# Kernel optimization log

Hardware: AMD Instinct MI355X
Metric: run time of the kernel (lower is better)

## Reference

```python
import jax, jax.numpy as jnp
import numpy as np


def setup_inputs() -> dict:
    key = jax.random.key(0)
    k0, k1, k2, k3 = jax.random.split(key, 4)
    B, T, C, H = 4, 4096, 1024, 64
    input_val = jax.random.normal(k0, (B, T, C), dtype=jnp.float32)
    scale = 0.02
    Wq = jax.random.normal(k1, (H, C), dtype=jnp.float32) * scale
    Wk = jax.random.normal(k2, (H, C), dtype=jnp.float32) * scale
    Wv = jax.random.normal(k3, (H, C), dtype=jnp.float32) * scale
    k_mask = jnp.ones((B, T), dtype=jnp.int32)
    return {"input_val": input_val, "Wq": Wq, "Wk": Wk, "Wv": Wv, "k_mask": k_mask}


def reference(input_val, Wq, Wk, Wv, k_mask):
    # input_val: [B, T, C]; Wq/Wk/Wv: [H, C] (torch Linear weight layout)
    B, T, C = input_val.shape
    H = Wq.shape[0]
    Q = input_val @ Wq.T  # [B, T, H]
    K = input_val @ Wk.T  # [B, T, H]
    V = input_val @ Wv.T  # [B, T, H]
    att = jnp.einsum('bqh,bkh->bqk', Q, K) / jnp.sqrt(jnp.asarray(H, input_val.dtype))
    neg_inf = jnp.asarray(-jnp.inf, att.dtype)
    # padding mask over keys: [B, 1, T]
    att = jnp.where(k_mask[:, None, :] == 0, neg_inf, att)
    # causal mask (rebuilt each call in the original)
    causal = jnp.tril(jnp.ones((T, T), dtype=bool))
    att = jnp.where(causal[None, :, :], att, neg_inf)
    att = jax.nn.softmax(att, axis=-1)
    return att @ V  # [B, T, H]
```

## Files before the change

kernel.cpp:

```cpp
#include <hip/hip_runtime.h>

typedef unsigned short u16;
typedef unsigned int u32;
typedef __attribute__((ext_vector_type(4))) float f32x4;
typedef __attribute__((ext_vector_type(8))) short s16x8;
typedef __attribute__((ext_vector_type(4))) int i32x4;
typedef __attribute__((ext_vector_type(2))) u32 u32x2;

#define TT 4096
#define NEG_BIG (-3.0e38f)

__device__ __forceinline__ u16 f2bf(float x){
  u32 u = __builtin_bit_cast(u32, x);
  u32 r = (u + 0x7FFFu + ((u >> 16) & 1u)) >> 16;
  return (u16)r;
}
__device__ __forceinline__ u32 pk2(float a, float b){
  return (u32)f2bf(a) | ((u32)f2bf(b) << 16);
}
__device__ __forceinline__ f32x4 mfma16(s16x8 a, s16x8 b, f32x4 c){
  return __builtin_amdgcn_mfma_f32_16x16x32_bf16(a, b, c, 0, 0, 0);
}

__global__ __launch_bounds__(256) void wconv_k(const float* __restrict__ Wq,
                                               const float* __restrict__ Wk,
                                               const float* __restrict__ Wv,
                                               u16* __restrict__ Wb){
  int i = blockIdx.x * 256 + threadIdx.x;
  float v;
  if (i < 65536)       v = Wq[i] * 0.125f;
  else if (i < 131072) v = Wk[i - 65536];
  else                 v = Wv[i - 131072];
  Wb[i] = f2bf(v);
}

__global__ __launch_bounds__(256) void qkv_k(const float* __restrict__ X,
                                             const u16* __restrict__ Wb,
                                             u16* __restrict__ Qb,
                                             u16* __restrict__ Kb,
                                             u16* __restrict__ Vt){
  __shared__ u16 Xs[32][40];
  const int tid = threadIdx.x;
  const int lane = tid & 63;
  const int wid = tid >> 6;
  const int q4 = lane & 15, g = lane >> 4;
  const int row0 = blockIdx.x * 32;
  const int b = row0 >> 12;
  const int trow = row0 & 4095;
  const int srow = tid >> 3, spart = tid & 7;
  const float* xsrc = X + (size_t)(row0 + srow) * 1024 + spart * 4;
  f32x4 c0 = *(const f32x4*)(xsrc);
  f32x4 acc[3][2];
  #pragma unroll
  for (int ci = 0; ci < 3; ++ci)
    #pragma unroll
    for (int tt = 0; tt < 2; ++tt) acc[ci][tt] = (f32x4){0.f, 0.f, 0.f, 0.f};
  const int ct0 = wid * 3;

  for (int kc = 0; kc < 32; ++kc){
    s16x8 wf[3];
    #pragma unroll
    for (int ci = 0; ci < 3; ++ci){
      int ct = ct0 + ci;
      wf[ci] = *(const s16x8*)(Wb + (size_t)(ct * 16 + q4) * 1024 + kc * 32 + g * 8);
    }
    const float* nx = xsrc + (kc < 31 ? (kc + 1) * 32 : 0);
    f32x4 n0 = *(const f32x4*)(nx);
    u32x2 wv;
    wv[0] = pk2(c0[0], c0[1]); wv[1] = pk2(c0[2], c0[3]);
    *(u32x2*)&Xs[srow][spart * 4] = wv;
    __syncthreads();
    s16x8 xf[2];
    #pragma unroll
    for (int tt = 0; tt < 2; ++tt) xf[tt] = *(const s16x8*)&Xs[tt * 16 + q4][g * 8];
    #pragma unroll
    for (int ci = 0; ci < 3; ++ci){
      #pragma unroll
      for (int tt = 0; tt < 2; ++tt){
        if (ct0 + ci < 8) acc[ci][tt] = mfma16(wf[ci], xf[tt], acc[ci][tt]);
        else              acc[ci][tt] = mfma16(xf[tt], wf[ci], acc[ci][tt]);
      }
    }
    __syncthreads();
    c0 = n0;
  }
  #pragma unroll
  for (int ci = 0; ci < 3; ++ci){
    int ct = ct0 + ci;
    #pragma unroll
    for (int tt = 0; tt < 2; ++tt){
      f32x4 v = acc[ci][tt];
      u32x2 pw; pw[0] = pk2(v[0], v[1]); pw[1] = pk2(v[2], v[3]);
      if (ct < 8){
        u16* dst = (ct < 4 ? Qb : Kb) + (size_t)(row0 + tt * 16 + q4) * 64 + (ct & 3) * 16 + g * 4;
        *(u32x2*)dst = pw;
      } else {
        u16* dst = Vt + (size_t)(b * 64 + (ct - 8) * 16 + q4) * TT + trow + tt * 16 + g * 4;
        *(u32x2*)dst = pw;
      }
    }
  }
}

__global__ __launch_bounds__(512, 4) void attn_k(const u16* __restrict__ Qb,
                                                 const u16* __restrict__ Kb,
                                                 const u16* __restrict__ Vt,
                                                 const int* __restrict__ km,
                                                 float* __restrict__ out){
  __shared__ u16 Plds[8][16][72];
  __shared__ float Part[2][4][16][68];
  __shared__ float Pml[2][4][2][16];
  const int tid = threadIdx.x;
  const int wid = tid >> 6;
  const int lane = tid & 63;
  const int q4 = lane & 15, g = lane >> 4;
  const int b = blockIdx.x >> 7;
  const int p = blockIdx.x & 127;
  const int si = wid & 1;
  const int qt = wid >> 1;

  const int s = (si == 0) ? p : 255 - p;
  const int qbase = s * 16;
  const int q_lane = qbase + q4;
  const int ntiles = (s >> 2) + 1;
  const int t0 = (ntiles * qt) >> 2;
  const int t1 = (ntiles * (qt + 1)) >> 2;
  const u16* qptr = Qb + (size_t)(b * TT + qbase + q4) * 64 + g * 8;
  const s16x8 qf0 = *(const s16x8*)(qptr);
  const s16x8 qf1 = *(const s16x8*)(qptr + 32);
  float m = NEG_BIG, l = 0.f;
  f32x4 o[4];
  #pragma unroll
  for (int ht = 0; ht < 4; ++ht) o[ht] = (f32x4){0.f, 0.f, 0.f, 0.f};

  for (int kt = t0; kt < t1; ++kt){
    const int kb = kt * 64;
    const u16* kp = Kb + (size_t)(b * TT + kb + q4) * 64 + g * 8;
    s16x8 kf[4][2];
    #pragma unroll
    for (int mt = 0; mt < 4; ++mt){
      kf[mt][0] = *(const s16x8*)(kp + mt * 1024);
      kf[mt][1] = *(const s16x8*)(kp + mt * 1024 + 32);
    }
    f32x4 sA[4];
    #pragma unroll
    for (int mt = 0; mt < 4; ++mt){
      sA[mt] = mfma16(kf[mt][0], qf0, (f32x4){0.f, 0.f, 0.f, 0.f});
      sA[mt] = mfma16(kf[mt][1], qf1, sA[mt]);
    }
    #pragma unroll
    for (int mt = 0; mt < 4; ++mt){
      i32x4 mk = *(const i32x4*)(km + b * TT + kb + mt * 16 + g * 4);
      #pragma unroll
      for (int r = 0; r < 4; ++r) if (mk[r] == 0) sA[mt][r] = NEG_BIG;
    }
    if (kt == ntiles - 1){
      #pragma unroll
      for (int mt = 0; mt < 4; ++mt)
        #pragma unroll
        for (int r = 0; r < 4; ++r){
          int key = kb + mt * 16 + g * 4 + r;
          if (key > q_lane) sA[mt][r] = NEG_BIG;
        }
    }
    float vmax = NEG_BIG;
    #pragma unroll
    for (int mt = 0; mt < 4; ++mt)
      #pragma unroll
      for (int r = 0; r < 4; ++r) vmax = fmaxf(vmax, sA[mt][r]);
    vmax = fmaxf(vmax, __shfl_xor(vmax, 16));
    vmax = fmaxf(vmax, __shfl_xor(vmax, 32));
    const float mn = fmaxf(m, vmax);
    const float sc = __expf(m - mn);
    float ps = 0.f;
    #pragma unroll
    for (int mt = 0; mt < 4; ++mt){
      float e0 = __expf(sA[mt][0] - mn), e1 = __expf(sA[mt][1] - mn);
      float e2 = __expf(sA[mt][2] - mn), e3 = __expf(sA[mt][3] - mn);
      ps += (e0 + e1) + (e2 + e3);
      u32x2 pw; pw[0] = pk2(e0, e1); pw[1] = pk2(e2, e3);
      *(u32x2*)&Plds[wid][q4][mt * 16 + g * 4] = pw;
    }
    ps += __shfl_xor(ps, 16);
    ps += __shfl_xor(ps, 32);
    l = l * sc + ps;
    m = mn;
    #pragma unroll
    for (int ht = 0; ht < 4; ++ht) o[ht] *= sc;
    const s16x8 pf0 = *(const s16x8*)&Plds[wid][q4][g * 8];
    const s16x8 pf1 = *(const s16x8*)&Plds[wid][q4][32 + g * 8];
    const u16* vp = Vt + (size_t)(b * 64 + q4) * TT + kb + g * 8;
    #pragma unroll
    for (int ht = 0; ht < 4; ++ht){
      s16x8 vf0 = *(const s16x8*)(vp + (size_t)(ht * 16) * TT);
      s16x8 vf1 = *(const s16x8*)(vp + (size_t)(ht * 16) * TT + 32);
      o[ht] = mfma16(vf0, pf0, o[ht]);
      o[ht] = mfma16(vf1, pf1, o[ht]);
    }
  }
  #pragma unroll
  for (int ht = 0; ht < 4; ++ht) *(f32x4*)&Part[si][qt][q4][ht * 16 + g * 4] = o[ht];
  if (g == 0){ Pml[si][qt][0][q4] = m; Pml[si][qt][1][q4] = l; }
  __syncthreads();
  if (wid < 2){
    const int so = (wid == 0) ? p : 255 - p;
    float mm0 = Pml[wid][0][0][q4], mm1 = Pml[wid][1][0][q4];
    float mm2 = Pml[wid][2][0][q4], mm3 = Pml[wid][3][0][q4];
    float ll0 = Pml[wid][0][1][q4], ll1 = Pml[wid][1][1][q4];
    float ll2 = Pml[wid][2][1][q4], ll3 = Pml[wid][3][1][q4];
    const float mt_ = fmaxf(fmaxf(mm0, mm1), fmaxf(mm2, mm3));
    const float w0 = __expf(mm0 - mt_), w1 = __expf(mm1 - mt_);
    const float w2 = __expf(mm2 - mt_), w3 = __expf(mm3 - mt_);
    const float lt = ll0 * w0 + ll1 * w1 + ll2 * w2 + ll3 * w3;
    const float rl = 1.0f / lt;
    float* op = out + (size_t)(b * TT + so * 16 + q4) * 64;
    #pragma unroll
    for (int ht = 0; ht < 4; ++ht){
      f32x4 o0 = *(const f32x4*)&Part[wid][0][q4][ht * 16 + g * 4];
      f32x4 o1 = *(const f32x4*)&Part[wid][1][q4][ht * 16 + g * 4];
      f32x4 o2 = *(const f32x4*)&Part[wid][2][q4][ht * 16 + g * 4];
      f32x4 o3 = *(const f32x4*)&Part[wid][3][q4][ht * 16 + g * 4];
      f32x4 ov = (o0 * w0 + o1 * w1 + o2 * w2 + o3 * w3) * rl;
      *(f32x4*)(op + ht * 16 + g * 4) = ov;
    }
  }
}

extern "C" void kernel_launch(void* const* d_in, const int* in_sizes, int n_in,
                              void* d_out, int out_size, void* d_ws, size_t ws_size,
                              hipStream_t stream){
  const float* X  = (const float*)d_in[0];
  const float* Wq = (const float*)d_in[1];
  const float* Wk = (const float*)d_in[2];
  const float* Wv = (const float*)d_in[3];
  const int*   km = (const int*)d_in[4];
  float* out = (float*)d_out;
  u16* Qb = (u16*)d_ws;
  u16* Kb = Qb + (size_t)16384 * 64;
  u16* Vt = Kb + (size_t)16384 * 64;
  u16* Wb = Vt + (size_t)16384 * 64;
  hipLaunchKernelGGL(wconv_k, dim3(768), dim3(256), 0, stream, Wq, Wk, Wv, Wb);
  hipLaunchKernelGGL(qkv_k,   dim3(512), dim3(256), 0, stream, X, Wb, Qb, Kb, Vt);
  hipLaunchKernelGGL(attn_k,  dim3(512), dim3(512), 0, stream, Qb, Kb, Vt, km, out);
}
```

Before: 192.5 us.

## Halve QKV tile rows, double-buffer LDS, and prefetch K/V tiles in attention

The QKV projection now processes 16 rows per block instead of 32 and launches twice as many blocks. It double-buffers the X staging tile in LDS so each iteration needs one barrier instead of two, and it prefetches the weight fragments one K-chunk ahead. In the attention kernel, the next K tile is software-pipelined into registers, and the V fragments and mask are loaded before the score MFMAs so global latency overlaps compute. The cost is higher register pressure in attention, and twice the weight-fragment traffic in QKV because each weight chunk is now reused across 16 rows instead of 32.

```diff
diff --git a/kernel.cpp b/kernel.cpp
--- a/kernel.cpp
+++ b/kernel.cpp
@@ -2,6 +2,7 @@
 
 typedef unsigned short u16;
 typedef unsigned int u32;
+typedef __attribute__((ext_vector_type(2))) float f32x2;
 typedef __attribute__((ext_vector_type(4))) float f32x4;
 typedef __attribute__((ext_vector_type(8))) short s16x8;
 typedef __attribute__((ext_vector_type(4))) int i32x4;
@@ -39,65 +40,53 @@
                                              u16* __restrict__ Qb,
                                              u16* __restrict__ Kb,
                                              u16* __restrict__ Vt){
-  __shared__ u16 Xs[32][40];
+  __shared__ u16 Xs[2][16][40];
   const int tid = threadIdx.x;
   const int lane = tid & 63;
   const int wid = tid >> 6;
   const int q4 = lane & 15, g = lane >> 4;
-  const int row0 = blockIdx.x * 32;
+  const int row0 = blockIdx.x * 16;
   const int b = row0 >> 12;
   const int trow = row0 & 4095;
-  const int srow = tid >> 3, spart = tid & 7;
-  const float* xsrc = X + (size_t)(row0 + srow) * 1024 + spart * 4;
-  f32x4 c0 = *(const f32x4*)(xsrc);
-  f32x4 acc[3][2];
+  const int srow = tid >> 4, spart = tid & 15;
+  const float* xsrc = X + (size_t)(row0 + srow) * 1024 + spart * 2;
+  f32x2 c0 = *(const f32x2*)(xsrc);
+  f32x4 acc[3];
+  #pragma unroll
+  for (int ci = 0; ci < 3; ++ci) acc[ci] = (f32x4){0.f, 0.f, 0.f, 0.f};
+  const int ct0 = wid * 3;
+  s16x8 wf[3];
   #pragma unroll
   for (int ci = 0; ci < 3; ++ci)
-    #pragma unroll
-    for (int tt = 0; tt < 2; ++tt) acc[ci][tt] = (f32x4){0.f, 0.f, 0.f, 0.f};
-  const int ct0 = wid * 3;
+    wf[ci] = *(const s16x8*)(Wb + (size_t)((ct0 + ci) * 16 + q4) * 1024 + g * 8);
 
   for (int kc = 0; kc < 32; ++kc){
-    s16x8 wf[3];
+    *(u32*)&Xs[kc & 1][srow][spart * 2] = pk2(c0[0], c0[1]);
+    __syncthreads();
+    if (kc < 31) c0 = *(const f32x2*)(xsrc + (kc + 1) * 32);
+    s16x8 xf = *(const s16x8*)&Xs[kc & 1][q4][g * 8];
     #pragma unroll
     for (int ci = 0; ci < 3; ++ci){
-      int ct = ct0 + ci;
-      wf[ci] = *(const s16x8*)(Wb + (size_t)(ct * 16 + q4) * 1024 + kc * 32 + g * 8);
-    }
-    const float* nx = xsrc + (kc < 31 ? (kc + 1) * 32 : 0);
-    f32x4 n0 = *(const f32x4*)(nx);
-    u32x2 wv;
-    wv[0] = pk2(c0[0], c0[1]); wv[1] = pk2(c0[2], c0[3]);
-    *(u32x2*)&Xs[srow][spart * 4] = wv;
-    __syncthreads();
-    s16x8 xf[2];
-    #pragma unroll
-    for (int tt = 0; tt < 2; ++tt) xf[tt] = *(const s16x8*)&Xs[tt * 16 + q4][g * 8];
-    #pragma unroll
-    for (int ci = 0; ci < 3; ++ci){
-      #pragma unroll
-      for (int tt = 0; tt < 2; ++tt){
-        if (ct0 + ci < 8) acc[ci][tt] = mfma16(wf[ci], xf[tt], acc[ci][tt]);
-        else              acc[ci][tt] = mfma16(xf[tt], wf[ci], acc[ci][tt]);
-      }
-    }
-    __syncthreads();
-    c0 = n0;
+      if (ct0 + ci < 8) acc[ci] = mfma16(wf[ci], xf, acc[ci]);
+      else              acc[ci] = mfma16(xf, wf[ci], acc[ci]);
+    }
+    if (kc < 31){
+      #pragma unroll
+      for (int ci = 0; ci < 3; ++ci)
+        wf[ci] = *(const s16x8*)(Wb + (size_t)((ct0 + ci) * 16 + q4) * 1024 + (kc + 1) * 32 + g * 8);
+    }
   }
   #pragma unroll
   for (int ci = 0; ci < 3; ++ci){
     int ct = ct0 + ci;
-    #pragma unroll
-    for (int tt = 0; tt < 2; ++tt){
-      f32x4 v = acc[ci][tt];
-      u32x2 pw; pw[0] = pk2(v[0], v[1]); pw[1] = pk2(v[2], v[3]);
-      if (ct < 8){
-        u16* dst = (ct < 4 ? Qb : Kb) + (size_t)(row0 + tt * 16 + q4) * 64 + (ct & 3) * 16 + g * 4;
-        *(u32x2*)dst = pw;
-      } else {
-        u16* dst = Vt + (size_t)(b * 64 + (ct - 8) * 16 + q4) * TT + trow + tt * 16 + g * 4;
-        *(u32x2*)dst = pw;
-      }
+    f32x4 v = acc[ci];
+    u32x2 pw; pw[0] = pk2(v[0], v[1]); pw[1] = pk2(v[2], v[3]);
+    if (ct < 8){
+      u16* dst = (ct < 4 ? Qb : Kb) + (size_t)(row0 + q4) * 64 + (ct & 3) * 16 + g * 4;
+      *(u32x2*)dst = pw;
+    } else {
+      u16* dst = Vt + (size_t)(b * 64 + (ct - 8) * 16 + q4) * TT + trow + g * 4;
+      *(u32x2*)dst = pw;
     }
   }
 }
@@ -133,69 +122,86 @@
   #pragma unroll
   for (int ht = 0; ht < 4; ++ht) o[ht] = (f32x4){0.f, 0.f, 0.f, 0.f};
 
-  for (int kt = t0; kt < t1; ++kt){
-    const int kb = kt * 64;
-    const u16* kp = Kb + (size_t)(b * TT + kb + q4) * 64 + g * 8;
-    s16x8 kf[4][2];
-    #pragma unroll
-    for (int mt = 0; mt < 4; ++mt){
-      kf[mt][0] = *(const s16x8*)(kp + mt * 1024);
-      kf[mt][1] = *(const s16x8*)(kp + mt * 1024 + 32);
-    }
-    f32x4 sA[4];
-    #pragma unroll
-    for (int mt = 0; mt < 4; ++mt){
-      sA[mt] = mfma16(kf[mt][0], qf0, (f32x4){0.f, 0.f, 0.f, 0.f});
-      sA[mt] = mfma16(kf[mt][1], qf1, sA[mt]);
-    }
-    #pragma unroll
-    for (int mt = 0; mt < 4; ++mt){
-      i32x4 mk = *(const i32x4*)(km + b * TT + kb + mt * 16 + g * 4);
-      #pragma unroll
-      for (int r = 0; r < 4; ++r) if (mk[r] == 0) sA[mt][r] = NEG_BIG;
-    }
-    if (kt == ntiles - 1){
+  if (t0 < t1){
+    s16x8 kf0[4], kf1[4];
+    {
+      const u16* kp = Kb + (size_t)(b * TT + t0 * 64 + q4) * 64 + g * 8;
+      #pragma unroll
+      for (int mt = 0; mt < 4; ++mt){
+        kf0[mt] = *(const s16x8*)(kp + mt * 1024);
+        kf1[mt] = *(const s16x8*)(kp + mt * 1024 + 32);
+      }
+    }
+    for (int kt = t0; kt < t1; ++kt){
+      const int kb = kt * 64;
+      const u16* vp = Vt + (size_t)(b * 64 + q4) * TT + kb + g * 8;
+      s16x8 vf0[4], vf1[4];
+      #pragma unroll
+      for (int ht = 0; ht < 4; ++ht) vf0[ht] = *(const s16x8*)(vp + (size_t)(ht * 16) * TT);
+      i32x4 mk[4];
+      #pragma unroll
+      for (int mt = 0; mt < 4; ++mt) mk[mt] = *(const i32x4*)(km + b * TT + kb + mt * 16 + g * 4);
+      f32x4 sA[4];
+      #pragma unroll
+      for (int mt = 0; mt < 4; ++mt){
+        sA[mt] = mfma16(kf0[mt], qf0, (f32x4){0.f, 0.f, 0.f, 0.f});
+        sA[mt] = mfma16(kf1[mt], qf1, sA[mt]);
+      }
+      #pragma unroll
+      for (int ht = 0; ht < 4; ++ht) vf1[ht] = *(const s16x8*)(vp + (size_t)(ht * 16) * TT + 32);
+      if (kt + 1 < t1){
+        const u16* kp = Kb + (size_t)(b * TT + kb + 64 + q4) * 64 + g * 8;
+        #pragma unroll
+        for (int mt = 0; mt < 4; ++mt){
+          kf0[mt] = *(const s16x8*)(kp + mt * 1024);
+          kf1[mt] = *(const s16x8*)(kp + mt * 1024 + 32);
+        }
+      }
+      #pragma unroll
+      for (int mt = 0; mt < 4; ++mt){
+        #pragma unroll
+        for (int r = 0; r < 4; ++r) if (mk[mt][r] == 0) sA[mt][r] = NEG_BIG;
+      }
+      if (kt == ntiles - 1){
+        #pragma unroll
+        for (int mt = 0; mt < 4; ++mt)
+          #pragma unroll
+          for (int r = 0; r < 4; ++r){
+            int key = kb + mt * 16 + g * 4 + r;
+            if (key > q_lane) sA[mt][r] = NEG_BIG;
+          }
+      }
+      float vmax = NEG_BIG;
       #pragma unroll
       for (int mt = 0; mt < 4; ++mt)
         #pragma unroll
-        for (int r = 0; r < 4; ++r){
-          int key = kb + mt * 16 + g * 4 + r;
-          if (key > q_lane) sA[mt][r] = NEG_BIG;
-        }
-    }
-    float vmax = NEG_BIG;
-    #pragma unroll
-    for (int mt = 0; mt < 4; ++mt)
-      #pragma unroll
-      for (int r = 0; r < 4; ++r) vmax = fmaxf(vmax, sA[mt][r]);
-    vmax = fmaxf(vmax, __shfl_xor(vmax, 16));
-    vmax = fmaxf(vmax, __shfl_xor(vmax, 32));
-    const float mn = fmaxf(m, vmax);
-    const float sc = __expf(m - mn);
-    float ps = 0.f;
-    #pragma unroll
-    for (int mt = 0; mt < 4; ++mt){
-      float e0 = __expf(sA[mt][0] - mn), e1 = __expf(sA[mt][1] - mn);
-      float e2 = __expf(sA[mt][2] - mn), e3 = __expf(sA[mt][3] - mn);
-      ps += (e0 + e1) + (e2 + e3);
-      u32x2 pw; pw[0] = pk2(e0, e1); pw[1] = pk2(e2, e3);
-      *(u32x2*)&Plds[wid][q4][mt * 16 + g * 4] = pw;
-    }
-    ps += __shfl_xor(ps, 16);
-    ps += __shfl_xor(ps, 32);
-    l = l * sc + ps;
-    m = mn;
-    #pragma unroll
-    for (int ht = 0; ht < 4; ++ht) o[ht] *= sc;
-    const s16x8 pf0 = *(const s16x8*)&Plds[wid][q4][g * 8];
-    const s16x8 pf1 = *(const s16x8*)&Plds[wid][q4][32 + g * 8];
-    const u16* vp = Vt + (size_t)(b * 64 + q4) * TT + kb + g * 8;
-    #pragma unroll
-    for (int ht = 0; ht < 4; ++ht){
-      s16x8 vf0 = *(const s16x8*)(vp + (size_t)(ht * 16) * TT);
-      s16x8 vf1 = *(const s16x8*)(vp + (size_t)(ht * 16) * TT + 32);
-      o[ht] = mfma16(vf0, pf0, o[ht]);
-      o[ht] = mfma16(vf1, pf1, o[ht]);
+        for (int r = 0; r < 4; ++r) vmax = fmaxf(vmax, sA[mt][r]);
+      vmax = fmaxf(vmax, __shfl_xor(vmax, 16));
+      vmax = fmaxf(vmax, __shfl_xor(vmax, 32));
+      const float mn = fmaxf(m, vmax);
+      const float sc = __expf(m - mn);
+      float ps = 0.f;
+      #pragma unroll
+      for (int mt = 0; mt < 4; ++mt){
+        float e0 = __expf(sA[mt][0] - mn), e1 = __expf(sA[mt][1] - mn);
+        float e2 = __expf(sA[mt][2] - mn), e3 = __expf(sA[mt][3] - mn);
+        ps += (e0 + e1) + (e2 + e3);
+        u32x2 pw; pw[0] = pk2(e0, e1); pw[1] = pk2(e2, e3);
+        *(u32x2*)&Plds[wid][q4][mt * 16 + g * 4] = pw;
+      }
+      ps += __shfl_xor(ps, 16);
+      ps += __shfl_xor(ps, 32);
+      l = l * sc + ps;
+      m = mn;
+      #pragma unroll
+      for (int ht = 0; ht < 4; ++ht) o[ht] *= sc;
+      const s16x8 pf0 = *(const s16x8*)&Plds[wid][q4][g * 8];
+      const s16x8 pf1 = *(const s16x8*)&Plds[wid][q4][32 + g * 8];
+      #pragma unroll
+      for (int ht = 0; ht < 4; ++ht){
+        o[ht] = mfma16(vf0[ht], pf0, o[ht]);
+        o[ht] = mfma16(vf1[ht], pf1, o[ht]);
+      }
     }
   }
   #pragma unroll
@@ -239,7 +245,7 @@
   u16* Kb = Qb + (size_t)16384 * 64;
   u16* Vt = Kb + (size_t)16384 * 64;
   u16* Wb = Vt + (size_t)16384 * 64;
-  hipLaunchKernelGGL(wconv_k, dim3(768), dim3(256), 0, stream, Wq, Wk, Wv, Wb);
-  hipLaunchKernelGGL(qkv_k,   dim3(512), dim3(256), 0, stream, X, Wb, Qb, Kb, Vt);
-  hipLaunchKernelGGL(attn_k,  dim3(512), dim3(512), 0, stream, Qb, Kb, Vt, km, out);
-}
+  hipLaunchKernelGGL(wconv_k, dim3(768),  dim3(256), 0, stream, Wq, Wk, Wv, Wb);
+  hipLaunchKernelGGL(qkv_k,   dim3(1024), dim3(256), 0, stream, X, Wb, Qb, Kb, Vt);
+  hipLaunchKernelGGL(attn_k,  dim3(512),  dim3(512), 0, stream, Qb, Kb, Vt, km, out);
+}
```

Measured after the change: 246.5 us. 1.28x slower.
